# Optimization experiments

Measured on AMD Instinct MI355X. Metric: run time of the kernel, lower is better.

Reference implementation:

```python
import jax, jax.numpy as jnp
import numpy as np

EPS = 1e-5
SLOPE = 0.01  # LeakyReLU default negative_slope


def conv3(x, w):
    # x: [B,C,D,H,W], w: [O,I,3,3,3]; SubMConv3d on a dense grid == dense SAME conv, no bias
    return jax.lax.conv_general_dilated(
        x, w, window_strides=(1, 1, 1), padding='SAME',
        dimension_numbers=('NCDHW', 'OIDHW', 'NCDHW'))


def bn_c(x, g, b, m, v):
    # BatchNorm1d (eval) over channel axis 1 of [B,C,D,H,W]
    s = (1.0, -1, 1, 1, 1)
    return (x - m.reshape(1, -1, 1, 1, 1)) * (g.reshape(1, -1, 1, 1, 1) * jax.lax.rsqrt(v.reshape(1, -1, 1, 1, 1) + EPS)) + b.reshape(1, -1, 1, 1, 1)


def bn_f(x, g, b, m, v):
    # BatchNorm1d (eval) over last (feature) axis
    return (x - m) * (g * jax.lax.rsqrt(v + EPS)) + b


def lrelu(x):
    return jnp.where(x > 0, x, SLOPE * x)


def setup_inputs() -> dict:
    key = jax.random.key(0)
    ks = jax.random.split(key, 32)
    B, C, D, H, W = 2, 256, 64, 64, 16
    N = 100000
    init_size, emb = 32, 3

    fea = jax.random.normal(ks[0], (B, C, D, H, W), dtype=jnp.float32)
    gi0 = jax.random.randint(ks[1], (B, N), 0, D)
    gi1 = jax.random.randint(ks[2], (B, N), 0, H)
    gi2 = jax.random.randint(ks[3], (B, N), 0, W)
    grid_ind = jnp.stack([gi0, gi1, gi2], axis=-1).astype(jnp.int32)  # [B,N,3]
    xyz = jax.random.normal(ks[4], (B, N, 3), dtype=jnp.float32)

    def bn_params(k, c):
        k1, k2, k3, k4 = jax.random.split(k, 4)
        return (1.0 + 0.1 * jax.random.normal(k1, (c,), jnp.float32),
                0.1 * jax.random.normal(k2, (c,), jnp.float32),
                0.1 * jax.random.normal(k3, (c,), jnp.float32),
                0.5 + jax.random.uniform(k4, (c,), jnp.float32))

    W1 = jax.random.normal(ks[5], (C, C, 3, 3, 3), jnp.float32) * (1.0 / np.sqrt(27 * C))
    g1, b1, m1, v1 = bn_params(ks[6], C)
    W2 = jax.random.normal(ks[7], (2 * init_size, C, 3, 3, 3), jnp.float32) * (1.0 / np.sqrt(27 * C))
    g2, b2, m2, v2 = bn_params(ks[8], 2 * init_size)
    W3 = jax.random.normal(ks[9], (init_size, 2 * init_size, 3, 3, 3), jnp.float32) * (1.0 / np.sqrt(27 * 2 * init_size))
    g3, b3, m3, v3 = bn_params(ks[10], init_size)

    Wo1 = jax.random.normal(ks[11], (init_size + 3, init_size), jnp.float32) * (1.0 / np.sqrt(init_size + 3))
    bo1 = 0.01 * jax.random.normal(ks[12], (init_size,), jnp.float32)
    go, bo, mo, vo = bn_params(ks[13], init_size)
    Wo2 = jax.random.normal(ks[14], (init_size, emb), jnp.float32) * (1.0 / np.sqrt(init_size))
    bo2 = 0.01 * jax.random.normal(ks[15], (emb,), jnp.float32)

    return dict(fea=fea, grid_ind=grid_ind, xyz=xyz,
                W1=W1, g1=g1, b1=b1, m1=m1, v1=v1,
                W2=W2, g2=g2, b2=b2, m2=m2, v2=v2,
                W3=W3, g3=g3, b3=b3, m3=m3, v3=v3,
                Wo1=Wo1, bo1=bo1, go=go, bo=bo, mo=mo, vo=vo,
                Wo2=Wo2, bo2=bo2)


def reference(fea, grid_ind, xyz,
              W1, g1, b1, m1, v1,
              W2, g2, b2, m2, v2,
              W3, g3, b3, m3, v3,
              Wo1, bo1, go, bo, mo, vo,
              Wo2, bo2):
    # sparse conv stack (dense-grid equivalent)
    x = lrelu(bn_c(conv3(fea, W1), g1, b1, m1, v1))
    x = lrelu(bn_c(conv3(x, W2), g2, b2, m2, v2))
    x = lrelu(bn_c(conv3(x, W3), g3, b3, m3, v3))  # [B, init_size, D, H, W]

    # fea.dense().permute(0,2,3,4,1) -> [B, D, H, W, C]; per-point gather
    xg = jnp.transpose(x, (0, 2, 3, 4, 1))
    B = xg.shape[0]
    bidx = jnp.arange(B)[:, None]  # [B,1]
    pt = xg[bidx, grid_ind[:, :, 0], grid_ind[:, :, 1], grid_ind[:, :, 2]]  # [B, N, init_size]

    # concat xyz, Linear -> BN -> ReLU -> Linear
    h = jnp.concatenate([pt, xyz[:, :, :3]], axis=-1)
    h = jax.nn.relu(bn_f(h @ Wo1 + bo1, go, bo, mo, vo))
    return h @ Wo2 + bo2  # [B, N, embedding_dim]
```

## Files before the change

### kernel.cpp

```cpp
#include <hip/hip_runtime.h>
#include <stdint.h>

#define EPS 1e-5f
#define SLOPE 0.01f

typedef short bf16x8 __attribute__((ext_vector_type(8)));
typedef float f32x4 __attribute__((ext_vector_type(4)));

__device__ __forceinline__ uint16_t f2bf(float x) {
  union { float f; uint32_t u; } v; v.f = x;
  return (uint16_t)((v.u + 0x7fffu + ((v.u >> 16) & 1u)) >> 16);
}

__device__ __forceinline__ void g2lds16(const void* g, void* l) {
  __builtin_amdgcn_global_load_lds(
      (const __attribute__((address_space(1))) void*)g,
      (__attribute__((address_space(3))) void*)l, 16, 0, 0);
}

__device__ __forceinline__ void vmwait(int n) {
  switch (n) {
    case 0:  asm volatile("s_waitcnt vmcnt(0)"  ::: "memory"); return;
    case 1:  asm volatile("s_waitcnt vmcnt(1)"  ::: "memory"); return;
    case 2:  asm volatile("s_waitcnt vmcnt(2)"  ::: "memory"); return;
    case 3:  asm volatile("s_waitcnt vmcnt(3)"  ::: "memory"); return;
    case 4:  asm volatile("s_waitcnt vmcnt(4)"  ::: "memory"); return;
    case 5:  asm volatile("s_waitcnt vmcnt(5)"  ::: "memory"); return;
    case 6:  asm volatile("s_waitcnt vmcnt(6)"  ::: "memory"); return;
    case 7:  asm volatile("s_waitcnt vmcnt(7)"  ::: "memory"); return;
    case 8:  asm volatile("s_waitcnt vmcnt(8)"  ::: "memory"); return;
    case 9:  asm volatile("s_waitcnt vmcnt(9)"  ::: "memory"); return;
    case 10: asm volatile("s_waitcnt vmcnt(10)" ::: "memory"); return;
    case 11: asm volatile("s_waitcnt vmcnt(11)" ::: "memory"); return;
    default: asm volatile("s_waitcnt vmcnt(12)" ::: "memory"); return;
  }
}

__device__ __forceinline__ void bar() {
  __builtin_amdgcn_sched_barrier(0);
  __builtin_amdgcn_s_barrier();
  __builtin_amdgcn_sched_barrier(0);
  asm volatile("" ::: "memory");
}

__global__ void prep_bn(const float* g1, const float* b1, const float* m1, const float* v1,
                        const float* g2, const float* b2, const float* m2, const float* v2,
                        const float* g3, const float* b3, const float* m3, const float* v3,
                        const float* go, const float* bo, const float* mo, const float* vo,
                        const float* bo1,
                        float* s1, float* be1, float* s2, float* be2,
                        float* s3, float* be3, float* so, float* beo) {
  int t = threadIdx.x;
  if (t < 256) { float s = g1[t] / sqrtf(v1[t] + EPS); s1[t] = s; be1[t] = b1[t] - m1[t] * s; }
  if (t < 64)  { float s = g2[t] / sqrtf(v2[t] + EPS); s2[t] = s; be2[t] = b2[t] - m2[t] * s; }
  if (t < 32)  { float s = g3[t] / sqrtf(v3[t] + EPS); s3[t] = s; be3[t] = b3[t] - m3[t] * s; }
  if (t < 32)  { float s = go[t] / sqrtf(vo[t] + EPS); so[t] = s; beo[t] = bo[t] + (bo1[t] - mo[t]) * s; }
}

__global__ void wtrans(const float* __restrict__ W, uint16_t* __restrict__ Wt,
                       int CO, int CI) {
  int idx = blockIdx.x * 256 + threadIdx.x;
  int total = CO * CI * 27;
  if (idx >= total) return;
  int t = idx / (CO * CI);
  int rem = idx % (CO * CI);
  int co = rem / CI, ci = rem % CI;
  Wt[idx] = f2bf(W[((size_t)co * CI + ci) * 27 + t]);
}

template <int C>
__global__ __launch_bounds__(256) void halo_zero(uint16_t* __restrict__ pad) {
  int id = blockIdx.x;
  int h = id % 66;
  int d = (id / 66) % 66;
  int b = id / (66 * 66);
  uint16_t* row = pad + ((size_t)b * 78408 + (size_t)(d * 1188 + h * 18)) * C;
  int tid = threadIdx.x;
  const uint4 z = make_uint4(0, 0, 0, 0);
  if (d == 0 || d == 65 || h == 0 || h == 65) {
    constexpr int n4 = 18 * C / 8;
    for (int i = tid; i < n4; i += 256) ((uint4*)row)[i] = z;
  } else {
    constexpr int n4 = C / 8;
    if (tid < n4) ((uint4*)row)[tid] = z;
    else if (tid < 2 * n4) ((uint4*)(row + 17 * C))[tid - n4] = z;
  }
}

__global__ __launch_bounds__(256) void transpose_fea(const float* __restrict__ fea,
                                                     uint16_t* __restrict__ pad0) {
  int tid = threadIdx.x;
  int idx = blockIdx.x;
  int half = idx & 1;
  int q = (idx >> 1) & 3;
  int d = (idx >> 3) & 63;
  int b = idx >> 9;
  int s = q * 256 + tid;
  int h = s >> 4, w = s & 15;
  const float* src = fea + (size_t)(b * 256 + half * 128) * 65536 + (size_t)d * 1024 + s;
  uint16_t* dst = pad0 + ((size_t)b * 78408 +
                          (size_t)((d + 1) * 1188 + (h + 1) * 18 + (w + 1))) * 256 + half * 128;
#pragma unroll 4
  for (int c8 = 0; c8 < 16; ++c8) {
    uint16_t v[8];
#pragma unroll
    for (int j = 0; j < 8; ++j)
      v[j] = f2bf(src[(size_t)(c8 * 8 + j) * 65536]);
    *(uint4*)&dst[c8 * 8] = *(uint4*)v;
  }
}

template <int CI, int CO, int MH, int WM, int WN, bool LAST>
__global__ __launch_bounds__(256, 2) void conv_mfma(const uint16_t* __restrict__ padIn,
                                                    const uint16_t* __restrict__ Wt,
                                                    const float* __restrict__ bnS,
                                                    const float* __restrict__ bnB,
                                                    uint16_t* __restrict__ padOut,
                                                    float* __restrict__ x3out) {
  constexpr int NTILE = CO;
  constexpr int MTILE = MH * 16;
  constexpr int MPW = MTILE / WM;
  constexpr int NPW = NTILE / WN;
  constexpr int MSUB = MPW / 16;
  constexpr int NSUB = NPW / 16;
  constexpr int KC = CI / 64;
  constexpr int G = 9 * KC;
  constexpr int HB = 64 / MH;
  constexpr int HALF = MH / 8;
  constexpr int ROWSTR = 18 * CI;

  __shared__ __align__(16) uint16_t Alds[2][18 * MH * 64];
  __shared__ __align__(16) uint16_t Blds[2][NTILE * 32];

  const int tid = threadIdx.x;
  const int lane = tid & 63;
  const int wv = tid >> 6;
  const int wvm = wv / WN;
  const int wvn = wv % WN;
  const int col = lane & 15;
  const int quad = lane >> 4;

  const int mt = blockIdx.x;
  const int b = mt / (64 * HB);
  const int r = mt % (64 * HB);
  const int d = r / HB;
  const int h0 = (r % HB) * MH;

  const size_t bOffIn = (size_t)b * 78408 * CI;

  const int qB = tid & 7;
  const int rB = ((tid >> 3) << 1) + (qB >> 2);
  const int uB = (qB & 3) ^ ((tid >> 3) & 3);

  const int aslot0 = wv * 5 - (wv >= 2 ? (wv - 2) : 0);
  const int anslots = (wv < 2) ? 5 : 4;

  const int aInstr = anslots * HALF;
  const int bInstr = (CO >= 64) ? (CO / 64) : ((wv * 64 < CO * 4) ? 1 : 0);

  auto stageA = [&](int dh, int kc, int as) {
    const int kd = dh / 3, kh = dh % 3;
    const uint16_t* agBase = padIn + bOffIn +
        (size_t)((d + kd) * 1188 + (h0 + kh) * 18) * CI + kc * 64 +
        (size_t)(lane >> 3) * ROWSTR;
    for (int p = 0; p < anslots; ++p) {
      int wp = aslot0 + p;
      int gu = (lane & 7) ^ (wp & 7);
#pragma unroll
      for (int hf = 0; hf < HALF; ++hf)
        g2lds16(agBase + (size_t)(hf * 8) * ROWSTR + wp * CI + gu * 8,
                (char*)Alds[as] + wp * (MH * 128) + hf * 1024);
    }
  };

  auto stageB = [&](int dh, int kc, int kw, int ks) {
    const uint16_t* bg = Wt + (size_t)((dh * 3 + kw) * CO) * CI + kc * 64 + ks * 32 + uB * 8;
    if constexpr (CO >= 64) {
#pragma unroll
      for (int p = 0; p < CO / 64; ++p)
        g2lds16(bg + (size_t)(rB + 64 * p) * CI, (char*)Blds[ks] + p * 4096 + wv * 1024);
    } else {
      if (tid < CO * 4)
        g2lds16(bg + (size_t)rB * CI, (char*)Blds[ks] + wv * 1024);
    }
  };

  f32x4 acc[MSUB][NSUB] = {};
  int acur = 0;

  auto compute = [&](int kw, int ks) {
    bf16x8 af[MSUB], bfr[NSUB];
#pragma unroll
    for (int mi = 0; mi < MSUB; ++mi) {
      int wq = col + kw;
      int u = (ks * 4 + quad) ^ (wq & 7);
      int mhIdx = wvm * MSUB + mi;
      af[mi] = *(const bf16x8*)&Alds[acur][wq * (MH * 64) + mhIdx * 64 + u * 8];
    }
#pragma unroll
    for (int ni = 0; ni < NSUB; ++ni) {
      int rw = wvn * NPW + ni * 16 + col;
      int u = quad ^ ((rw >> 1) & 3);
      bfr[ni] = *(const bf16x8*)&Blds[ks][(rw >> 1) * 64 + (rw & 1) * 32 + u * 8];
    }
    __builtin_amdgcn_s_setprio(1);
#pragma unroll
    for (int mi = 0; mi < MSUB; ++mi)
#pragma unroll
      for (int ni = 0; ni < NSUB; ++ni)
        acc[mi][ni] = __builtin_amdgcn_mfma_f32_16x16x32_bf16(af[mi], bfr[ni], acc[mi][ni], 0, 0, 0);
    __builtin_amdgcn_s_setprio(0);
  };

  stageA(0, 0, 0);
  stageB(0, 0, 0, 0);

  for (int g = 0; g < G; ++g) {
    const int dh = g / KC, kc = g % KC;
    const bool more = (g + 1 < G);
    const int dhn = (kc == KC - 1) ? dh + 1 : dh;
    const int kcn = (kc == KC - 1) ? 0 : kc + 1;
#pragma unroll
    for (int s = 0; s < 6; ++s) {
      const int kw = s >> 1, ks = s & 1;
      int issued = 0;
      if (s < 5) { stageB(dh, kc, (s + 1) >> 1, (s + 1) & 1); issued = bInstr; }
      else if (more) { stageB(dhn, kcn, 0, 0); issued = bInstr; }
      if (s == 4 && more) { stageA(dhn, kcn, acur ^ 1); issued += aInstr; }
      vmwait(issued + ((s == 5 && more) ? aInstr : 0));
      bar();
      compute(kw, ks);
      bar();
    }
    acur ^= 1;
  }

#pragma unroll
  for (int ni = 0; ni < NSUB; ++ni) {
    const int co = wvn * NPW + ni * 16 + col;
    const float sv = bnS[co];
    const float bv = bnB[co];
#pragma unroll
    for (int mi = 0; mi < MSUB; ++mi) {
#pragma unroll
      for (int rr = 0; rr < 4; ++rr) {
        int m = wvm * MPW + mi * 16 + quad * 4 + rr;
        float v = acc[mi][ni][rr] * sv + bv;
        v = v > 0.f ? v : SLOPE * v;
        int mh = m >> 4, w = m & 15;
        if (!LAST) {
          size_t o = ((size_t)b * 78408 +
                      (size_t)((d + 1) * 1188 + (h0 + mh + 1) * 18 + (w + 1))) * CO + co;
          padOut[o] = f2bf(v);
        } else {
          size_t o = ((size_t)b * 65536 + (size_t)((d * 64 + h0 + mh) * 16 + w)) * 32 + co;
          x3out[o] = v;
        }
      }
    }
  }
}

__global__ __launch_bounds__(256) void gather_mlp(const float* __restrict__ x3,
                                                  const int* __restrict__ gidx,
                                                  const float* __restrict__ xyz,
                                                  const float* __restrict__ Wo1,
                                                  const float* __restrict__ so,
                                                  const float* __restrict__ beo,
                                                  const float* __restrict__ Wo2,
                                                  const float* __restrict__ bo2,
                                                  float* __restrict__ out) {
  __shared__ __align__(16) float w1[35 * 32];
  __shared__ float w2[32 * 3];
  __shared__ float sS[32], sB[32], b2s[3];
  int tid = threadIdx.x;
  for (int i = tid; i < 1120; i += 256) w1[i] = Wo1[i];
  if (tid < 96) w2[tid] = Wo2[tid];
  if (tid < 32) { sS[tid] = so[tid]; sB[tid] = beo[tid]; }
  if (tid < 3) b2s[tid] = bo2[tid];
  __syncthreads();

  int idx = blockIdx.x * 256 + tid;
  if (idx >= 200000) return;
  int b = idx >= 100000 ? 1 : 0;
  int gb = idx * 3;
  int i0 = gidx[gb], i1 = gidx[gb + 1], i2 = gidx[gb + 2];
  const float* pt = x3 + ((size_t)b * 65536 + (size_t)((i0 * 64 + i1) * 16 + i2)) * 32;

  float h[35];
#pragma unroll
  for (int q = 0; q < 8; ++q) {
    float4 v = *(const float4*)(pt + q * 4);
    h[q * 4] = v.x; h[q * 4 + 1] = v.y; h[q * 4 + 2] = v.z; h[q * 4 + 3] = v.w;
  }
  h[32] = xyz[gb]; h[33] = xyz[gb + 1]; h[34] = xyz[gb + 2];

  float a[32];
#pragma unroll
  for (int j = 0; j < 32; ++j) a[j] = 0.f;
#pragma unroll
  for (int k = 0; k < 35; ++k) {
    float hk = h[k];
    const float4* wr = (const float4*)(w1 + k * 32);
#pragma unroll
    for (int q = 0; q < 8; ++q) {
      float4 wv = wr[q];
      a[q * 4 + 0] += hk * wv.x;
      a[q * 4 + 1] += hk * wv.y;
      a[q * 4 + 2] += hk * wv.z;
      a[q * 4 + 3] += hk * wv.w;
    }
  }
  float o0 = b2s[0], o1 = b2s[1], o2 = b2s[2];
#pragma unroll
  for (int j = 0; j < 32; ++j) {
    float y = a[j] * sS[j] + sB[j];
    y = y > 0.f ? y : 0.f;
    o0 += y * w2[j * 3 + 0];
    o1 += y * w2[j * 3 + 1];
    o2 += y * w2[j * 3 + 2];
  }
  out[gb] = o0; out[gb + 1] = o1; out[gb + 2] = o2;
}

extern "C" void kernel_launch(void* const* d_in, const int* in_sizes, int n_in,
                              void* d_out, int out_size, void* d_ws, size_t ws_size,
                              hipStream_t stream) {
  (void)in_sizes; (void)n_in; (void)out_size;
  if (ws_size < 165130000) return;

  const float* fea = (const float*)d_in[0];
  const int*   gidx = (const int*)d_in[1];
  const float* xyz = (const float*)d_in[2];
  const float* W1 = (const float*)d_in[3];
  const float* g1 = (const float*)d_in[4];
  const float* b1 = (const float*)d_in[5];
  const float* m1 = (const float*)d_in[6];
  const float* v1 = (const float*)d_in[7];
  const float* W2 = (const float*)d_in[8];
  const float* g2 = (const float*)d_in[9];
  const float* b2 = (const float*)d_in[10];
  const float* m2 = (const float*)d_in[11];
  const float* v2 = (const float*)d_in[12];
  const float* W3 = (const float*)d_in[13];
  const float* g3 = (const float*)d_in[14];
  const float* b3 = (const float*)d_in[15];
  const float* m3 = (const float*)d_in[16];
  const float* v3 = (const float*)d_in[17];
  const float* Wo1 = (const float*)d_in[18];
  const float* bo1 = (const float*)d_in[19];
  const float* go = (const float*)d_in[20];
  const float* bo = (const float*)d_in[21];
  const float* mo = (const float*)d_in[22];
  const float* vo = (const float*)d_in[23];
  const float* Wo2 = (const float*)d_in[24];
  const float* bo2 = (const float*)d_in[25];

  char* ws = (char*)d_ws;
  uint16_t* pad0 = (uint16_t*)(ws);
  uint16_t* pad1 = (uint16_t*)(ws + 80289792);
  uint16_t* Wt1 = (uint16_t*)(ws + 160579584);
  uint16_t* Wt2 = (uint16_t*)(ws + 164118528);
  uint16_t* Wt3 = (uint16_t*)(ws + 165003264);
  float* s1  = (float*)(ws + 165113856 + 0 * 1024);
  float* be1 = (float*)(ws + 165113856 + 1 * 1024);
  float* s2  = (float*)(ws + 165113856 + 2 * 1024);
  float* be2 = (float*)(ws + 165113856 + 3 * 1024);
  float* s3  = (float*)(ws + 165113856 + 4 * 1024);
  float* be3 = (float*)(ws + 165113856 + 5 * 1024);
  float* so  = (float*)(ws + 165113856 + 6 * 1024);
  float* beo = (float*)(ws + 165113856 + 7 * 1024);
  uint16_t* pad2 = (uint16_t*)(ws);
  float* x3 = (float*)(ws + 20072448);

  prep_bn<<<1, 256, 0, stream>>>(g1, b1, m1, v1, g2, b2, m2, v2, g3, b3, m3, v3,
                                 go, bo, mo, vo, bo1, s1, be1, s2, be2, s3, be3, so, beo);
  wtrans<<<6912, 256, 0, stream>>>(W1, Wt1, 256, 256);
  wtrans<<<1728, 256, 0, stream>>>(W2, Wt2, 64, 256);
  wtrans<<<216, 256, 0, stream>>>(W3, Wt3, 32, 64);
  halo_zero<256><<<17424, 256, 0, stream>>>(pad0);
  transpose_fea<<<1024, 256, 0, stream>>>(fea, pad0);

  conv_mfma<256, 256, 8, 2, 2, false>
      <<<1024, 256, 0, stream>>>(pad0, Wt1, s1, be1, pad1, nullptr);

  halo_zero<64><<<8712, 256, 0, stream>>>(pad2);

  conv_mfma<256, 64, 16, 4, 1, false>
      <<<512, 256, 0, stream>>>(pad1, Wt2, s2, be2, pad2, nullptr);

  conv_mfma<64, 32, 16, 4, 1, true>
      <<<512, 256, 0, stream>>>(pad2, Wt3, s3, be3, nullptr, x3);

  gather_mlp<<<782, 256, 0, stream>>>(x3, gidx, xyz, Wo1, so, beo, Wo2, bo2, (float*)d_out);
}
```

Baseline: 1.134 ms.

## Double conv tile sizes to 512-thread blocks and triple-buffer weight staging

The conv kernels move to 8-wave, 512-thread blocks with twice as many output rows per block (MH 8→16 for conv1, 16→32 for conv2/3). Weight slices are now triple-buffered and prefetched two steps ahead. LDS fragment reads are issued before the vmcnt wait and barrier, so they overlap with outstanding global loads. The aim is more operand reuse per weight load and better latency hiding, at the cost of larger LDS use and register pressure that may cut occupancy and wave count per CU.

Result: slower. 1.257 ms (+10.9%).

```diff
diff --git a/kernel.cpp b/kernel.cpp
--- a/kernel.cpp
+++ b/kernel.cpp
@@ -32,7 +32,11 @@
     case 9:  asm volatile("s_waitcnt vmcnt(9)"  ::: "memory"); return;
     case 10: asm volatile("s_waitcnt vmcnt(10)" ::: "memory"); return;
     case 11: asm volatile("s_waitcnt vmcnt(11)" ::: "memory"); return;
-    default: asm volatile("s_waitcnt vmcnt(12)" ::: "memory"); return;
+    case 12: asm volatile("s_waitcnt vmcnt(12)" ::: "memory"); return;
+    case 13: asm volatile("s_waitcnt vmcnt(13)" ::: "memory"); return;
+    case 14: asm volatile("s_waitcnt vmcnt(14)" ::: "memory"); return;
+    case 15: asm volatile("s_waitcnt vmcnt(15)" ::: "memory"); return;
+    default: asm volatile("s_waitcnt vmcnt(16)" ::: "memory"); return;
   }
 }
 
@@ -111,12 +115,13 @@
 }
 
 template <int CI, int CO, int MH, int WM, int WN, bool LAST>
-__global__ __launch_bounds__(256, 2) void conv_mfma(const uint16_t* __restrict__ padIn,
+__global__ __launch_bounds__(512, 2) void conv_mfma(const uint16_t* __restrict__ padIn,
                                                     const uint16_t* __restrict__ Wt,
                                                     const float* __restrict__ bnS,
                                                     const float* __restrict__ bnB,
                                                     uint16_t* __restrict__ padOut,
                                                     float* __restrict__ x3out) {
+  constexpr int WAVES = WM * WN;
   constexpr int NTILE = CO;
   constexpr int MTILE = MH * 16;
   constexpr int MPW = MTILE / WM;
@@ -128,9 +133,11 @@
   constexpr int HB = 64 / MH;
   constexpr int HALF = MH / 8;
   constexpr int ROWSTR = 18 * CI;
+  constexpr int PASSROWS = 128;
+  constexpr int ABASE = 18 / WAVES, AREM = 18 % WAVES;
 
   __shared__ __align__(16) uint16_t Alds[2][18 * MH * 64];
-  __shared__ __align__(16) uint16_t Blds[2][NTILE * 32];
+  __shared__ __align__(16) uint16_t Blds[3][NTILE * 32];
 
   const int tid = threadIdx.x;
   const int lane = tid & 63;
@@ -148,17 +155,18 @@
 
   const size_t bOffIn = (size_t)b * 78408 * CI;
 
-  const int qB = tid & 7;
-  const int rB = ((tid >> 3) << 1) + (qB >> 2);
-  const int uB = (qB & 3) ^ ((tid >> 3) & 3);
-
-  const int aslot0 = wv * 5 - (wv >= 2 ? (wv - 2) : 0);
-  const int anslots = (wv < 2) ? 5 : 4;
-
+  const int jB = tid & 7;
+  const int rB = ((tid >> 3) << 1) + (jB >> 2);
+  const int uB = (jB & 3) ^ ((tid >> 3) & 3);
+
+  const int aslot0 = (wv < AREM) ? wv * (ABASE + 1)
+                                 : AREM * (ABASE + 1) + (wv - AREM) * ABASE;
+  const int anslots = (wv < AREM) ? ABASE + 1 : ABASE;
   const int aInstr = anslots * HALF;
-  const int bInstr = (CO >= 64) ? (CO / 64) : ((wv * 64 < CO * 4) ? 1 : 0);
-
-  auto stageA = [&](int dh, int kc, int as) {
+  const int bInstr = (CO >= PASSROWS) ? (CO / PASSROWS) : ((wv * 64 < CO * 4) ? 1 : 0);
+
+  auto stageA = [&](int g, int as) {
+    const int dh = g / KC, kc = g % KC;
     const int kd = dh / 3, kh = dh % 3;
     const uint16_t* agBase = padIn + bOffIn +
         (size_t)((d + kd) * 1188 + (h0 + kh) * 18) * CI + kc * 64 +
@@ -173,63 +181,68 @@
     }
   };
 
-  auto stageB = [&](int dh, int kc, int kw, int ks) {
+  auto stageB = [&](int g, int s, int bi) {
+    const int dh = g / KC, kc = g % KC;
+    const int kw = s >> 1, ks = s & 1;
     const uint16_t* bg = Wt + (size_t)((dh * 3 + kw) * CO) * CI + kc * 64 + ks * 32 + uB * 8;
-    if constexpr (CO >= 64) {
-#pragma unroll
-      for (int p = 0; p < CO / 64; ++p)
-        g2lds16(bg + (size_t)(rB + 64 * p) * CI, (char*)Blds[ks] + p * 4096 + wv * 1024);
+    if constexpr (CO >= PASSROWS) {
+#pragma unroll
+      for (int p = 0; p < CO / PASSROWS; ++p)
+        g2lds16(bg + (size_t)(rB + PASSROWS * p) * CI,
+                (char*)Blds[bi] + p * (PASSROWS * 64) + wv * 1024);
     } else {
       if (tid < CO * 4)
-        g2lds16(bg + (size_t)rB * CI, (char*)Blds[ks] + wv * 1024);
+        g2lds16(bg + (size_t)rB * CI, (char*)Blds[bi] + wv * 1024);
     }
   };
 
   f32x4 acc[MSUB][NSUB] = {};
   int acur = 0;
 
-  auto compute = [&](int kw, int ks) {
-    bf16x8 af[MSUB], bfr[NSUB];
-#pragma unroll
-    for (int mi = 0; mi < MSUB; ++mi) {
-      int wq = col + kw;
-      int u = (ks * 4 + quad) ^ (wq & 7);
-      int mhIdx = wvm * MSUB + mi;
-      af[mi] = *(const bf16x8*)&Alds[acur][wq * (MH * 64) + mhIdx * 64 + u * 8];
-    }
-#pragma unroll
-    for (int ni = 0; ni < NSUB; ++ni) {
-      int rw = wvn * NPW + ni * 16 + col;
-      int u = quad ^ ((rw >> 1) & 3);
-      bfr[ni] = *(const bf16x8*)&Blds[ks][(rw >> 1) * 64 + (rw & 1) * 32 + u * 8];
-    }
-    __builtin_amdgcn_s_setprio(1);
-#pragma unroll
-    for (int mi = 0; mi < MSUB; ++mi)
-#pragma unroll
-      for (int ni = 0; ni < NSUB; ++ni)
-        acc[mi][ni] = __builtin_amdgcn_mfma_f32_16x16x32_bf16(af[mi], bfr[ni], acc[mi][ni], 0, 0, 0);
-    __builtin_amdgcn_s_setprio(0);
-  };
-
-  stageA(0, 0, 0);
-  stageB(0, 0, 0, 0);
+  stageA(0, 0);
+  stageB(0, 0, 0);
+  stageB(0, 1, 1);
+  vmwait(bInstr);
+  bar();
 
   for (int g = 0; g < G; ++g) {
-    const int dh = g / KC, kc = g % KC;
     const bool more = (g + 1 < G);
-    const int dhn = (kc == KC - 1) ? dh + 1 : dh;
-    const int kcn = (kc == KC - 1) ? 0 : kc + 1;
 #pragma unroll
     for (int s = 0; s < 6; ++s) {
       const int kw = s >> 1, ks = s & 1;
-      int issued = 0;
-      if (s < 5) { stageB(dh, kc, (s + 1) >> 1, (s + 1) & 1); issued = bInstr; }
-      else if (more) { stageB(dhn, kcn, 0, 0); issued = bInstr; }
-      if (s == 4 && more) { stageA(dhn, kcn, acur ^ 1); issued += aInstr; }
-      vmwait(issued + ((s == 5 && more) ? aInstr : 0));
+      constexpr int BI2[6] = {2, 0, 1, 2, 0, 1};
+      constexpr int BI[6]  = {0, 1, 2, 0, 1, 2};
+      if (s < 4) stageB(g, s + 2, BI2[s]);
+      else if (more) stageB(g + 1, s - 4, BI2[s]);
+      if (s == 4 && more) stageA(g + 1, acur ^ 1);
+      bf16x8 af[MSUB], bfr[NSUB];
+#pragma unroll
+      for (int mi = 0; mi < MSUB; ++mi) {
+        int wq = col + kw;
+        int u = (ks * 4 + quad) ^ (wq & 7);
+        int mhIdx = wvm * MSUB + mi;
+        af[mi] = *(const bf16x8*)&Alds[acur][wq * (MH * 64) + mhIdx * 64 + u * 8];
+      }
+#pragma unroll
+      for (int ni = 0; ni < NSUB; ++ni) {
+        int rw = wvn * NPW + ni * 16 + col;
+        int u = quad ^ ((rw >> 1) & 3);
+        bfr[ni] = *(const bf16x8*)&Blds[BI[s]][(rw >> 1) * 64 + (rw & 1) * 32 + u * 8];
+      }
+      {
+        int allow = 0;
+        if (s < 4 || more) allow += bInstr;
+        if (s == 4 && more) allow += aInstr;
+        vmwait(allow);
+      }
       bar();
-      compute(kw, ks);
+      __builtin_amdgcn_s_setprio(1);
+#pragma unroll
+      for (int mi = 0; mi < MSUB; ++mi)
+#pragma unroll
+        for (int ni = 0; ni < NSUB; ++ni)
+          acc[mi][ni] = __builtin_amdgcn_mfma_f32_16x16x32_bf16(af[mi], bfr[ni], acc[mi][ni], 0, 0, 0);
+      __builtin_amdgcn_s_setprio(0);
       bar();
     }
     acur ^= 1;
@@ -381,16 +394,16 @@
   halo_zero<256><<<17424, 256, 0, stream>>>(pad0);
   transpose_fea<<<1024, 256, 0, stream>>>(fea, pad0);
 
-  conv_mfma<256, 256, 8, 2, 2, false>
-      <<<1024, 256, 0, stream>>>(pad0, Wt1, s1, be1, pad1, nullptr);
+  conv_mfma<256, 256, 16, 2, 4, false>
+      <<<512, 512, 0, stream>>>(pad0, Wt1, s1, be1, pad1, nullptr);
 
   halo_zero<64><<<8712, 256, 0, stream>>>(pad2);
 
-  conv_mfma<256, 64, 16, 4, 1, false>
-      <<<512, 256, 0, stream>>>(pad1, Wt2, s2, be2, pad2, nullptr);
-
-  conv_mfma<64, 32, 16, 4, 1, true>
-      <<<512, 256, 0, stream>>>(pad2, Wt3, s3, be3, nullptr, x3);
+  conv_mfma<256, 64, 32, 8, 1, false>
+      <<<256, 512, 0, stream>>>(pad1, Wt2, s2, be2, pad2, nullptr);
+
+  conv_mfma<64, 32, 32, 8, 1, true>
+      <<<256, 512, 0, stream>>>(pad2, Wt3, s3, be3, nullptr, x3);
 
   gather_mlp<<<782, 256, 0, stream>>>(x3, gidx, xyz, Wo1, so, beo, Wo2, bo2, (float*)d_out);
 }
```
